# Kernel optimization log

Hardware: AMD Instinct MI355X
Metric: run time of the kernel (lower is better)

Reference implementation:

```python
import jax, jax.numpy as jnp
import numpy as np

N = 50000
E = 800000
IN_C, HID_C, OUT_C = 128, 128, 64


def setup_inputs() -> dict:
    key = jax.random.key(0)
    k_x, k_e, k_w1, k_w2 = jax.random.split(key, 4)
    x = jax.random.normal(k_x, (N, IN_C), dtype=jnp.float32)
    edge_index = jax.random.randint(k_e, (2, E), 0, N, dtype=jnp.int64)
    # glorot-ish init scale
    W1 = jax.random.normal(k_w1, (IN_C, HID_C), dtype=jnp.float32) * (1.0 / np.sqrt(IN_C))
    b1 = jnp.zeros((HID_C,), dtype=jnp.float32)
    W2 = jax.random.normal(k_w2, (HID_C, OUT_C), dtype=jnp.float32) * (1.0 / np.sqrt(HID_C))
    b2 = jnp.zeros((OUT_C,), dtype=jnp.float32)
    return {"x": x, "edge_index": edge_index, "W1": W1, "b1": b1, "W2": W2, "b2": b2}


def _gcn_norm(edge_index, num_nodes):
    # PyG gcn_norm with add_self_loops=True: deg over destination (col), sym norm
    loops = jnp.arange(num_nodes, dtype=edge_index.dtype)
    src = jnp.concatenate([edge_index[0], loops])
    dst = jnp.concatenate([edge_index[1], loops])
    deg = jax.ops.segment_sum(jnp.ones_like(dst, dtype=jnp.float32), dst, num_segments=num_nodes)
    dinv = jnp.where(deg > 0, jax.lax.rsqrt(deg), 0.0)
    norm = dinv[src] * dinv[dst]  # [E+N]
    return src, dst, norm


def _gcn_conv(x, src, dst, norm, W, b, num_nodes):
    h = x @ W                              # [N, out]
    msg = h[src] * norm[:, None]           # [E+N, out] gather + scale
    agg = jax.ops.segment_sum(msg, dst, num_segments=num_nodes)  # scatter-add
    return agg + b


def reference(x, edge_index, W1, b1, W2, b2):
    num_nodes = x.shape[0]
    src, dst, norm = _gcn_norm(edge_index, num_nodes)
    h = _gcn_conv(x, src, dst, norm, W1, b1, num_nodes)
    h = jax.nn.relu(h)
    out = _gcn_conv(h, src, dst, norm, W2, b2, num_nodes)
    return out
```

## Files before the change

### kernel.cpp

```cpp
#include <hip/hip_runtime.h>
#include <hip/hip_bf16.h>


#define IN_C 128
#define HID_C 128
#define OUT_C 64
#define BKT_SH 8
#define BKT_NODES 256
#define CHUNK 4096
#define CAPB 6144
#define OVF_CAP 65536

typedef float f32x4 __attribute__((ext_vector_type(4)));
typedef short bf16x8 __attribute__((ext_vector_type(8)));

__device__ inline unsigned short f2bf_rtn(float f) {
  unsigned u = __float_as_uint(f);
  unsigned r = u + 0x7fffu + ((u >> 16) & 1u);
  return (unsigned short)(r >> 16);
}
__device__ inline unsigned pack_bf2(float a, float b) {
  return (unsigned)f2bf_rtn(a) | ((unsigned)f2bf_rtn(b) << 16);
}

__global__ __launch_bounds__(256) void wt_zero_kernel(
    const float* __restrict__ W1, const float* __restrict__ W2,
    short* __restrict__ w1t, short* __restrict__ w2t,
    int* __restrict__ zbase, int zints) {
  int i = blockIdx.x * 256 + threadIdx.x;
  if (i < zints) zbase[i] = 0;
  if (i < IN_C * HID_C) {
    int n = i >> 7, k = i & 127;
    w1t[i] = (short)f2bf_rtn(W1[k * HID_C + n]);
  }
  if (i < HID_C * OUT_C) {
    int n = i >> 7, k = i & 127;
    w2t[i] = (short)f2bf_rtn(W2[k * OUT_C + n]);
  }
}

__global__ __launch_bounds__(256) void p1_gemm1_kernel(
    const int* __restrict__ ei, unsigned* __restrict__ pairs,
    int* __restrict__ bcnt, uint2* __restrict__ ovf, int* __restrict__ ovf_cnt,
    int* __restrict__ ovfb, int E, int K, int P1B,
    const float* __restrict__ X, const short* __restrict__ Wt,
    unsigned short* __restrict__ H, int ntiles) {
  int t = threadIdx.x;
  if ((int)blockIdx.x < P1B) {
    __shared__ unsigned buf[CHUNK];
    __shared__ int hist[256];
    __shared__ int lofs[256];
    __shared__ int cur[256];
    __shared__ int gbase[256];
    __shared__ int ws4[4];
    int base_e = blockIdx.x * CHUNK;
    int cnt_e = E - base_e;
    if (cnt_e > CHUNK) cnt_e = CHUNK;

    hist[t] = 0;
    __syncthreads();

    for (int i = t; i < cnt_e; i += 256)
      atomicAdd(&hist[ei[E + base_e + i] >> BKT_SH], 1);
    __syncthreads();

    int v = hist[t];
    int lane = t & 63, wid = t >> 6;
    int inc = v;
    #pragma unroll
    for (int off = 1; off < 64; off <<= 1) {
      int u = __shfl_up(inc, off, 64);
      if (lane >= off) inc += u;
    }
    if (lane == 63) ws4[wid] = inc;
    __syncthreads();
    if (t == 0) {
      int a = ws4[0], b = ws4[1], c = ws4[2];
      ws4[0] = 0; ws4[1] = a; ws4[2] = a + b; ws4[3] = a + b + c;
    }
    __syncthreads();
    int excl = ws4[wid] + inc - v;
    lofs[t] = excl;
    cur[t] = excl;
    if (t < K && v > 0) gbase[t] = atomicAdd(&bcnt[t], v);
    __syncthreads();

    for (int i = t; i < cnt_e; i += 256) {
      int src = ei[base_e + i];
      int dst = ei[E + base_e + i];
      int b = dst >> BKT_SH;
      int pos = atomicAdd(&cur[b], 1);
      buf[pos] = (unsigned)src | ((unsigned)(dst & (BKT_NODES - 1)) << 16) |
                 ((unsigned)b << 24);
    }
    __syncthreads();

    for (int i = t; i < cnt_e; i += 256) {
      unsigned w = buf[i];
      int b = w >> 24;
      int g = gbase[b] + (i - lofs[b]);
      if (g < CAPB) {
        pairs[(size_t)b * CAPB + g] = w;
      } else {
        int oi = atomicAdd(ovf_cnt, 1);
        if (oi < OVF_CAP) {
          unsigned dst = (unsigned)(b << BKT_SH) | ((w >> 16) & 0xFFu);
          ovf[oi] = make_uint2(w & 0xFFFFu, dst);
          atomicAdd(&ovfb[b], 1);
        }
      }
    }
  } else {
    int lane = t & 63;
    int tile = ((int)blockIdx.x - P1B) * 4 + (t >> 6);
    if (tile >= ntiles) return;
    constexpr int NT = HID_C / 16;

    int arow = tile * 16 + (lane & 15);
    int kch = (lane >> 4) * 8;

    bf16x8 afrag[4];
    const float4* Xf = (const float4*)X;
    #pragma unroll
    for (int kt = 0; kt < 4; ++kt) {
      float4 f0 = Xf[(size_t)arow * 32 + (kt * 32 + kch) / 4];
      float4 f1 = Xf[(size_t)arow * 32 + (kt * 32 + kch) / 4 + 1];
      bf16x8 a;
      a[0] = (short)f2bf_rtn(f0.x); a[1] = (short)f2bf_rtn(f0.y);
      a[2] = (short)f2bf_rtn(f0.z); a[3] = (short)f2bf_rtn(f0.w);
      a[4] = (short)f2bf_rtn(f1.x); a[5] = (short)f2bf_rtn(f1.y);
      a[6] = (short)f2bf_rtn(f1.z); a[7] = (short)f2bf_rtn(f1.w);
      afrag[kt] = a;
    }

    const bf16x8* W8 = (const bf16x8*)Wt;
    f32x4 zero = {0.f, 0.f, 0.f, 0.f};
    f32x4 acc[NT];
    #pragma unroll
    for (int ct = 0; ct < NT; ++ct) acc[ct] = zero;

    #pragma unroll
    for (int ct = 0; ct < NT; ++ct) {
      int bcol = ct * 16 + (lane & 15);
      #pragma unroll
      for (int kt = 0; kt < 4; ++kt) {
        bf16x8 b = W8[bcol * 16 + (kt * 32 + kch) / 8];
        acc[ct] = __builtin_amdgcn_mfma_f32_16x16x32_bf16(afrag[kt], b, acc[ct], 0, 0, 0);
      }
    }

    int r0 = tile * 16 + (lane >> 4) * 4;
    #pragma unroll
    for (int ct = 0; ct < NT; ++ct) {
      #pragma unroll
      for (int j = 0; j < 4; ++j)
        H[(size_t)(r0 + j) * HID_C + ct * 16 + (lane & 15)] = f2bf_rtn(acc[ct][j]);
    }
  }
}

__global__ __launch_bounds__(256) void phase2_csr_kernel(
    const unsigned* __restrict__ pairs, const int* __restrict__ bcnt,
    const int* __restrict__ ovfb, const uint2* __restrict__ ovf,
    const int* __restrict__ ovf_cnt, int* __restrict__ rowstart,
    float* __restrict__ dinv, unsigned short* __restrict__ csr, int N, int K) {
  int b = blockIdx.x;
  int t = threadIdx.x;
  __shared__ int hist[BKT_NODES];
  __shared__ int cur[BKT_NODES];
  __shared__ int sbase[256];
  __shared__ int ws4[4];
  int lane = t & 63, wid = t >> 6;

  int cb = 0;
  if (t < K) {
    int c = bcnt[t];
    cb = (c < CAPB ? c : CAPB) + ovfb[t];
  }
  {
    int inc = cb;
    #pragma unroll
    for (int off = 1; off < 64; off <<= 1) {
      int u = __shfl_up(inc, off, 64);
      if (lane >= off) inc += u;
    }
    if (lane == 63) ws4[wid] = inc;
    __syncthreads();
    if (t == 0) {
      int a = ws4[0], bb = ws4[1], c = ws4[2];
      ws4[0] = 0; ws4[1] = a; ws4[2] = a + bb; ws4[3] = a + bb + c;
    }
    __syncthreads();
    int excl = ws4[wid] + inc - cb;
    sbase[t] = excl;
    if (b == K - 1 && t == K - 1) rowstart[N] = excl + cb;
  }
  __syncthreads();
  int base = sbase[b];

  hist[t] = 0;
  __syncthreads();

  int cnt = bcnt[b];
  if (cnt > CAPB) cnt = CAPB;
  const unsigned* reg = pairs + (size_t)b * CAPB;

  for (int i = t; i < cnt; i += 256)
    atomicAdd(&hist[(reg[i] >> 16) & 0xFFu], 1);
  int oc = *ovf_cnt;
  if (oc > OVF_CAP) oc = OVF_CAP;
  for (int i = t; i < oc; i += 256) {
    uint2 p = ovf[i];
    if ((int)(p.y >> BKT_SH) == b) atomicAdd(&hist[p.y & (BKT_NODES - 1)], 1);
  }
  __syncthreads();

  int v = hist[t];
  int inc = v;
  #pragma unroll
  for (int off = 1; off < 64; off <<= 1) {
    int u = __shfl_up(inc, off, 64);
    if (lane >= off) inc += u;
  }
  __syncthreads();
  if (lane == 63) ws4[wid] = inc;
  __syncthreads();
  if (t == 0) {
    int a = ws4[0], bb = ws4[1], c = ws4[2];
    ws4[0] = 0; ws4[1] = a; ws4[2] = a + bb; ws4[3] = a + bb + c;
  }
  __syncthreads();
  int excl = ws4[wid] + inc - v;

  int node = b * BKT_NODES + t;
  if (node < N) {
    rowstart[node] = base + excl;
    dinv[node] = rsqrtf((float)(v + 1));
  }
  cur[t] = base + excl;
  __syncthreads();

  for (int i = t; i < cnt; i += 256) {
    unsigned w = reg[i];
    int pos = atomicAdd(&cur[(w >> 16) & 0xFFu], 1);
    csr[pos] = (unsigned short)(w & 0xffffu);
  }
  for (int i = t; i < oc; i += 256) {
    uint2 p = ovf[i];
    if ((int)(p.y >> BKT_SH) == b) {
      int pos = atomicAdd(&cur[p.y & (BKT_NODES - 1)], 1);
      csr[pos] = (unsigned short)p.x;
    }
  }
}

__global__ __launch_bounds__(256) void mfma_gemm2_kernel(
    const unsigned short* __restrict__ Xb16, const short* __restrict__ Wt,
    const float* __restrict__ dinv, unsigned short* __restrict__ H, int ntiles) {
  int lane = threadIdx.x & 63;
  int tile = blockIdx.x * 4 + (threadIdx.x >> 6);
  if (tile >= ntiles) return;
  constexpr int NT = OUT_C / 16;

  int arow = tile * 16 + (lane & 15);
  int kch = (lane >> 4) * 8;

  const bf16x8* Xb = (const bf16x8*)Xb16;
  bf16x8 afrag[4];
  #pragma unroll
  for (int kt = 0; kt < 4; ++kt)
    afrag[kt] = Xb[(size_t)arow * 16 + (kt * 32 + kch) / 8];

  const bf16x8* W8 = (const bf16x8*)Wt;
  f32x4 zero = {0.f, 0.f, 0.f, 0.f};
  f32x4 acc[NT];
  #pragma unroll
  for (int ct = 0; ct < NT; ++ct) acc[ct] = zero;

  #pragma unroll
  for (int ct = 0; ct < NT; ++ct) {
    int bcol = ct * 16 + (lane & 15);
    #pragma unroll
    for (int kt = 0; kt < 4; ++kt) {
      bf16x8 b = W8[bcol * 16 + (kt * 32 + kch) / 8];
      acc[ct] = __builtin_amdgcn_mfma_f32_16x16x32_bf16(afrag[kt], b, acc[ct], 0, 0, 0);
    }
  }

  int r0 = tile * 16 + (lane >> 4) * 4;
  float di[4];
  #pragma unroll
  for (int j = 0; j < 4; ++j) di[j] = dinv[r0 + j];
  #pragma unroll
  for (int ct = 0; ct < NT; ++ct) {
    #pragma unroll
    for (int j = 0; j < 4; ++j)
      H[(size_t)(r0 + j) * OUT_C + ct * 16 + (lane & 15)] = f2bf_rtn(acc[ct][j] * di[j]);
  }
}

template <int C, bool RELU, bool OUT_BF16, bool SRC_SCALE>
__global__ __launch_bounds__(256) void agg_bf16_kernel(
    const unsigned short* __restrict__ Hs, const int* __restrict__ rowstart,
    const unsigned short* __restrict__ csr, const float* __restrict__ dinv,
    const float* __restrict__ bias, void* __restrict__ out, int n) {
  constexpr int TPN = C / 8;
  constexpr int NPB = 256 / TPN;
  int lane = threadIdx.x % TPN;
  int node = blockIdx.x * NPB + threadIdx.x / TPN;
  if (node >= n) return;

  const uint4* H4 = reinterpret_cast<const uint4*>(Hs);
  int s = rowstart[node];
  int e = rowstart[node + 1];
  float dnode = dinv[node];

  float acc[8];
  {
    uint4 v = H4[(size_t)node * TPN + lane];
    float ds = SRC_SCALE ? dnode : 1.0f;
    acc[0] = __uint_as_float(v.x << 16) * ds;
    acc[1] = __uint_as_float(v.x & 0xffff0000u) * ds;
    acc[2] = __uint_as_float(v.y << 16) * ds;
    acc[3] = __uint_as_float(v.y & 0xffff0000u) * ds;
    acc[4] = __uint_as_float(v.z << 16) * ds;
    acc[5] = __uint_as_float(v.z & 0xffff0000u) * ds;
    acc[6] = __uint_as_float(v.w << 16) * ds;
    acc[7] = __uint_as_float(v.w & 0xffff0000u) * ds;
  }

  int p = s;
  for (; p + 1 < e; p += 2) {
    int s0 = csr[p];
    int s1 = csr[p + 1];
    uint4 v0 = H4[(size_t)s0 * TPN + lane];
    uint4 v1 = H4[(size_t)s1 * TPN + lane];
    if (SRC_SCALE) {
      float d0 = dinv[s0], d1 = dinv[s1];
      acc[0] = fmaf(__uint_as_float(v0.x << 16), d0, acc[0]);
      acc[1] = fmaf(__uint_as_float(v0.x & 0xffff0000u), d0, acc[1]);
      acc[2] = fmaf(__uint_as_float(v0.y << 16), d0, acc[2]);
      acc[3] = fmaf(__uint_as_float(v0.y & 0xffff0000u), d0, acc[3]);
      acc[4] = fmaf(__uint_as_float(v0.z << 16), d0, acc[4]);
      acc[5] = fmaf(__uint_as_float(v0.z & 0xffff0000u), d0, acc[5]);
      acc[6] = fmaf(__uint_as_float(v0.w << 16), d0, acc[6]);
      acc[7] = fmaf(__uint_as_float(v0.w & 0xffff0000u), d0, acc[7]);
      acc[0] = fmaf(__uint_as_float(v1.x << 16), d1, acc[0]);
      acc[1] = fmaf(__uint_as_float(v1.x & 0xffff0000u), d1, acc[1]);
      acc[2] = fmaf(__uint_as_float(v1.y << 16), d1, acc[2]);
      acc[3] = fmaf(__uint_as_float(v1.y & 0xffff0000u), d1, acc[3]);
      acc[4] = fmaf(__uint_as_float(v1.z << 16), d1, acc[4]);
      acc[5] = fmaf(__uint_as_float(v1.z & 0xffff0000u), d1, acc[5]);
      acc[6] = fmaf(__uint_as_float(v1.w << 16), d1, acc[6]);
      acc[7] = fmaf(__uint_as_float(v1.w & 0xffff0000u), d1, acc[7]);
    } else {
      acc[0] += __uint_as_float(v0.x << 16);
      acc[1] += __uint_as_float(v0.x & 0xffff0000u);
      acc[2] += __uint_as_float(v0.y << 16);
      acc[3] += __uint_as_float(v0.y & 0xffff0000u);
      acc[4] += __uint_as_float(v0.z << 16);
      acc[5] += __uint_as_float(v0.z & 0xffff0000u);
      acc[6] += __uint_as_float(v0.w << 16);
      acc[7] += __uint_as_float(v0.w & 0xffff0000u);
      acc[0] += __uint_as_float(v1.x << 16);
      acc[1] += __uint_as_float(v1.x & 0xffff0000u);
      acc[2] += __uint_as_float(v1.y << 16);
      acc[3] += __uint_as_float(v1.y & 0xffff0000u);
      acc[4] += __uint_as_float(v1.z << 16);
      acc[5] += __uint_as_float(v1.z & 0xffff0000u);
      acc[6] += __uint_as_float(v1.w << 16);
      acc[7] += __uint_as_float(v1.w & 0xffff0000u);
    }
  }
  if (p < e) {
    int s0 = csr[p];
    uint4 v0 = H4[(size_t)s0 * TPN + lane];
    float d0 = SRC_SCALE ? dinv[s0] : 1.0f;
    acc[0] = fmaf(__uint_as_float(v0.x << 16), d0, acc[0]);
    acc[1] = fmaf(__uint_as_float(v0.x & 0xffff0000u), d0, acc[1]);
    acc[2] = fmaf(__uint_as_float(v0.y << 16), d0, acc[2]);
    acc[3] = fmaf(__uint_as_float(v0.y & 0xffff0000u), d0, acc[3]);
    acc[4] = fmaf(__uint_as_float(v0.z << 16), d0, acc[4]);
    acc[5] = fmaf(__uint_as_float(v0.z & 0xffff0000u), d0, acc[5]);
    acc[6] = fmaf(__uint_as_float(v0.w << 16), d0, acc[6]);
    acc[7] = fmaf(__uint_as_float(v0.w & 0xffff0000u), d0, acc[7]);
  }

  float4 b0 = reinterpret_cast<const float4*>(bias)[lane * 2];
  float4 b1 = reinterpret_cast<const float4*>(bias)[lane * 2 + 1];
  float r[8];
  r[0] = fmaf(acc[0], dnode, b0.x);
  r[1] = fmaf(acc[1], dnode, b0.y);
  r[2] = fmaf(acc[2], dnode, b0.z);
  r[3] = fmaf(acc[3], dnode, b0.w);
  r[4] = fmaf(acc[4], dnode, b1.x);
  r[5] = fmaf(acc[5], dnode, b1.y);
  r[6] = fmaf(acc[6], dnode, b1.z);
  r[7] = fmaf(acc[7], dnode, b1.w);
  if (RELU) {
    #pragma unroll
    for (int j = 0; j < 8; ++j) r[j] = fmaxf(r[j], 0.f);
  }
  if (OUT_BF16) {
    uint4 o;
    o.x = pack_bf2(r[0], r[1]);
    o.y = pack_bf2(r[2], r[3]);
    o.z = pack_bf2(r[4], r[5]);
    o.w = pack_bf2(r[6], r[7]);
    reinterpret_cast<uint4*>(out)[(size_t)node * TPN + lane] = o;
  } else {
    float4* o4 = reinterpret_cast<float4*>(out) + (size_t)node * (C / 4);
    o4[lane * 2] = make_float4(r[0], r[1], r[2], r[3]);
    o4[lane * 2 + 1] = make_float4(r[4], r[5], r[6], r[7]);
  }
}

extern "C" void kernel_launch(void* const* d_in, const int* in_sizes, int n_in,
                              void* d_out, int out_size, void* d_ws, size_t ws_size,
                              hipStream_t stream) {
  const float* x  = (const float*)d_in[0];
  const int*   ei = (const int*)d_in[1];
  const float* W1 = (const float*)d_in[2];
  const float* b1 = (const float*)d_in[3];
  const float* W2 = (const float*)d_in[4];
  const float* b2 = (const float*)d_in[5];
  float* out = (float*)d_out;

  const int N = in_sizes[0] / IN_C;
  const int E = in_sizes[1] / 2;
  const int K = (N + BKT_NODES - 1) >> BKT_SH;
  const int NTILES = (N + 15) / 16;
  const int P1B = (E + CHUNK - 1) / CHUNK;
  const int GB1 = (NTILES + 3) / 4;

  char* ws = (char*)d_ws;
  size_t off = 0;
  auto alloc = [&](size_t bytes) -> void* {
    void* p = ws + off;
    off += (bytes + 255) & ~(size_t)255;
    return p;
  };
  int* bcnt    = (int*)alloc((size_t)K * 4);
  int* ovf_cnt = (int*)alloc(4);
  int* ovfb    = (int*)alloc((size_t)K * 4);
  size_t zero_bytes = off;
  const int zints = (int)(zero_bytes / 4);

  int*   rowstart    = (int*)  alloc((size_t)(N + 1) * 4);
  float* dinv        = (float*)alloc((size_t)N * 4);
  unsigned* pairs    = (unsigned*)alloc((size_t)K * CAPB * 4);
  uint2* ovf         = (uint2*)alloc((size_t)OVF_CAP * 8);
  unsigned short* csr = (unsigned short*)alloc((size_t)E * 2);
  unsigned short* hs  = (unsigned short*)alloc((size_t)N * HID_C * 2);
  unsigned short* x2  = (unsigned short*)alloc((size_t)N * HID_C * 2);
  short* w1t         = (short*)alloc((size_t)IN_C * HID_C * 2);
  short* w2t         = (short*)alloc((size_t)HID_C * OUT_C * 2);

  int wt_threads = zints > IN_C * HID_C ? zints : IN_C * HID_C;
  wt_zero_kernel<<<(wt_threads + 255) / 256, 256, 0, stream>>>(
      W1, W2, w1t, w2t, (int*)ws, zints);

  p1_gemm1_kernel<<<P1B + GB1, 256, 0, stream>>>(
      ei, pairs, bcnt, ovf, ovf_cnt, ovfb, E, K, P1B, x, w1t, hs, NTILES);

  phase2_csr_kernel<<<K, 256, 0, stream>>>(
      pairs, bcnt, ovfb, ovf, ovf_cnt, rowstart, dinv, csr, N, K);

  agg_bf16_kernel<HID_C, true, true, true><<<(N + 15) / 16, 256, 0, stream>>>(
      hs, rowstart, csr, dinv, b1, x2, N);

  mfma_gemm2_kernel<<<(NTILES + 3) / 4, 256, 0, stream>>>(
      x2, w2t, dinv, hs, NTILES);

  agg_bf16_kernel<OUT_C, false, false, false><<<(N + 31) / 32, 256, 0, stream>>>(
      hs, rowstart, csr, dinv, b2, out, N);
}
```

Baseline: 110.5 us.

## Fuse layer-1 aggregation with layer-2 MFMA GEMM via shared memory tile

Layer-1 aggregation (with ReLU and bias) now feeds a 16-row bf16 tile held in LDS directly into the layer-2 MFMA GEMM inside one kernel. This drops the N×128 bf16 intermediate write and read-back, plus one kernel launch. Each of the four waves computes one 16-column output tile. The cost is a block-wide sync after the irregular gather, so each block waits on its slowest node and the GEMM stage sees lower occupancy and latency hiding.

```diff
diff --git a/kernel.cpp b/kernel.cpp
--- a/kernel.cpp
+++ b/kernel.cpp
@@ -254,88 +254,45 @@
   }
 }
 
-__global__ __launch_bounds__(256) void mfma_gemm2_kernel(
-    const unsigned short* __restrict__ Xb16, const short* __restrict__ Wt,
-    const float* __restrict__ dinv, unsigned short* __restrict__ H, int ntiles) {
-  int lane = threadIdx.x & 63;
-  int tile = blockIdx.x * 4 + (threadIdx.x >> 6);
-  if (tile >= ntiles) return;
-  constexpr int NT = OUT_C / 16;
-
-  int arow = tile * 16 + (lane & 15);
-  int kch = (lane >> 4) * 8;
-
-  const bf16x8* Xb = (const bf16x8*)Xb16;
-  bf16x8 afrag[4];
-  #pragma unroll
-  for (int kt = 0; kt < 4; ++kt)
-    afrag[kt] = Xb[(size_t)arow * 16 + (kt * 32 + kch) / 8];
-
-  const bf16x8* W8 = (const bf16x8*)Wt;
-  f32x4 zero = {0.f, 0.f, 0.f, 0.f};
-  f32x4 acc[NT];
-  #pragma unroll
-  for (int ct = 0; ct < NT; ++ct) acc[ct] = zero;
-
-  #pragma unroll
-  for (int ct = 0; ct < NT; ++ct) {
-    int bcol = ct * 16 + (lane & 15);
-    #pragma unroll
-    for (int kt = 0; kt < 4; ++kt) {
-      bf16x8 b = W8[bcol * 16 + (kt * 32 + kch) / 8];
-      acc[ct] = __builtin_amdgcn_mfma_f32_16x16x32_bf16(afrag[kt], b, acc[ct], 0, 0, 0);
-    }
-  }
-
-  int r0 = tile * 16 + (lane >> 4) * 4;
-  float di[4];
-  #pragma unroll
-  for (int j = 0; j < 4; ++j) di[j] = dinv[r0 + j];
-  #pragma unroll
-  for (int ct = 0; ct < NT; ++ct) {
-    #pragma unroll
-    for (int j = 0; j < 4; ++j)
-      H[(size_t)(r0 + j) * OUT_C + ct * 16 + (lane & 15)] = f2bf_rtn(acc[ct][j] * di[j]);
-  }
-}
-
-template <int C, bool RELU, bool OUT_BF16, bool SRC_SCALE>
-__global__ __launch_bounds__(256) void agg_bf16_kernel(
+__global__ __launch_bounds__(256) void agg1_gemm2_kernel(
     const unsigned short* __restrict__ Hs, const int* __restrict__ rowstart,
     const unsigned short* __restrict__ csr, const float* __restrict__ dinv,
-    const float* __restrict__ bias, void* __restrict__ out, int n) {
-  constexpr int TPN = C / 8;
-  constexpr int NPB = 256 / TPN;
-  int lane = threadIdx.x % TPN;
-  int node = blockIdx.x * NPB + threadIdx.x / TPN;
-  if (node >= n) return;
-
-  const uint4* H4 = reinterpret_cast<const uint4*>(Hs);
-  int s = rowstart[node];
-  int e = rowstart[node + 1];
-  float dnode = dinv[node];
+    const float* __restrict__ b1, const short* __restrict__ w2t,
+    unsigned short* __restrict__ H2, int n) {
+  __shared__ unsigned x2s[16][64];
+  int t = threadIdx.x;
+  int row = t >> 4;
+  int lane16 = t & 15;
+  int node = blockIdx.x * 16 + row;
 
   float acc[8];
-  {
-    uint4 v = H4[(size_t)node * TPN + lane];
-    float ds = SRC_SCALE ? dnode : 1.0f;
-    acc[0] = __uint_as_float(v.x << 16) * ds;
-    acc[1] = __uint_as_float(v.x & 0xffff0000u) * ds;
-    acc[2] = __uint_as_float(v.y << 16) * ds;
-    acc[3] = __uint_as_float(v.y & 0xffff0000u) * ds;
-    acc[4] = __uint_as_float(v.z << 16) * ds;
-    acc[5] = __uint_as_float(v.z & 0xffff0000u) * ds;
-    acc[6] = __uint_as_float(v.w << 16) * ds;
-    acc[7] = __uint_as_float(v.w & 0xffff0000u) * ds;
-  }
-
-  int p = s;
-  for (; p + 1 < e; p += 2) {
-    int s0 = csr[p];
-    int s1 = csr[p + 1];
-    uint4 v0 = H4[(size_t)s0 * TPN + lane];
-    uint4 v1 = H4[(size_t)s1 * TPN + lane];
-    if (SRC_SCALE) {
+  #pragma unroll
+  for (int j = 0; j < 8; ++j) acc[j] = 0.f;
+
+  if (node < n) {
+    const uint4* H4 = reinterpret_cast<const uint4*>(Hs);
+    int s = rowstart[node];
+    int e = rowstart[node + 1];
+    float dnode = dinv[node];
+
+    {
+      uint4 v = H4[(size_t)node * 16 + lane16];
+      acc[0] = __uint_as_float(v.x << 16) * dnode;
+      acc[1] = __uint_as_float(v.x & 0xffff0000u) * dnode;
+      acc[2] = __uint_as_float(v.y << 16) * dnode;
+      acc[3] = __uint_as_float(v.y & 0xffff0000u) * dnode;
+      acc[4] = __uint_as_float(v.z << 16) * dnode;
+      acc[5] = __uint_as_float(v.z & 0xffff0000u) * dnode;
+      acc[6] = __uint_as_float(v.w << 16) * dnode;
+      acc[7] = __uint_as_float(v.w & 0xffff0000u) * dnode;
+    }
+
+    int p = s;
+    for (; p + 1 < e; p += 2) {
+      int s0 = csr[p];
+      int s1 = csr[p + 1];
+      uint4 v0 = H4[(size_t)s0 * 16 + lane16];
+      uint4 v1 = H4[(size_t)s1 * 16 + lane16];
       float d0 = dinv[s0], d1 = dinv[s1];
       acc[0] = fmaf(__uint_as_float(v0.x << 16), d0, acc[0]);
       acc[1] = fmaf(__uint_as_float(v0.x & 0xffff0000u), d0, acc[1]);
@@ -353,66 +310,134 @@
       acc[5] = fmaf(__uint_as_float(v1.z & 0xffff0000u), d1, acc[5]);
       acc[6] = fmaf(__uint_as_float(v1.w << 16), d1, acc[6]);
       acc[7] = fmaf(__uint_as_float(v1.w & 0xffff0000u), d1, acc[7]);
-    } else {
-      acc[0] += __uint_as_float(v0.x << 16);
-      acc[1] += __uint_as_float(v0.x & 0xffff0000u);
-      acc[2] += __uint_as_float(v0.y << 16);
-      acc[3] += __uint_as_float(v0.y & 0xffff0000u);
-      acc[4] += __uint_as_float(v0.z << 16);
-      acc[5] += __uint_as_float(v0.z & 0xffff0000u);
-      acc[6] += __uint_as_float(v0.w << 16);
-      acc[7] += __uint_as_float(v0.w & 0xffff0000u);
-      acc[0] += __uint_as_float(v1.x << 16);
-      acc[1] += __uint_as_float(v1.x & 0xffff0000u);
-      acc[2] += __uint_as_float(v1.y << 16);
-      acc[3] += __uint_as_float(v1.y & 0xffff0000u);
-      acc[4] += __uint_as_float(v1.z << 16);
-      acc[5] += __uint_as_float(v1.z & 0xffff0000u);
-      acc[6] += __uint_as_float(v1.w << 16);
-      acc[7] += __uint_as_float(v1.w & 0xffff0000u);
-    }
+    }
+    if (p < e) {
+      int s0 = csr[p];
+      uint4 v0 = H4[(size_t)s0 * 16 + lane16];
+      float d0 = dinv[s0];
+      acc[0] = fmaf(__uint_as_float(v0.x << 16), d0, acc[0]);
+      acc[1] = fmaf(__uint_as_float(v0.x & 0xffff0000u), d0, acc[1]);
+      acc[2] = fmaf(__uint_as_float(v0.y << 16), d0, acc[2]);
+      acc[3] = fmaf(__uint_as_float(v0.y & 0xffff0000u), d0, acc[3]);
+      acc[4] = fmaf(__uint_as_float(v0.z << 16), d0, acc[4]);
+      acc[5] = fmaf(__uint_as_float(v0.z & 0xffff0000u), d0, acc[5]);
+      acc[6] = fmaf(__uint_as_float(v0.w << 16), d0, acc[6]);
+      acc[7] = fmaf(__uint_as_float(v0.w & 0xffff0000u), d0, acc[7]);
+    }
+
+    const float4* b4 = reinterpret_cast<const float4*>(b1);
+    float4 bv0 = b4[lane16 * 2];
+    float4 bv1 = b4[lane16 * 2 + 1];
+    acc[0] = fmaxf(fmaf(acc[0], dnode, bv0.x), 0.f);
+    acc[1] = fmaxf(fmaf(acc[1], dnode, bv0.y), 0.f);
+    acc[2] = fmaxf(fmaf(acc[2], dnode, bv0.z), 0.f);
+    acc[3] = fmaxf(fmaf(acc[3], dnode, bv0.w), 0.f);
+    acc[4] = fmaxf(fmaf(acc[4], dnode, bv1.x), 0.f);
+    acc[5] = fmaxf(fmaf(acc[5], dnode, bv1.y), 0.f);
+    acc[6] = fmaxf(fmaf(acc[6], dnode, bv1.z), 0.f);
+    acc[7] = fmaxf(fmaf(acc[7], dnode, bv1.w), 0.f);
+  }
+
+  x2s[row][lane16 * 4 + 0] = pack_bf2(acc[0], acc[1]);
+  x2s[row][lane16 * 4 + 1] = pack_bf2(acc[2], acc[3]);
+  x2s[row][lane16 * 4 + 2] = pack_bf2(acc[4], acc[5]);
+  x2s[row][lane16 * 4 + 3] = pack_bf2(acc[6], acc[7]);
+  __syncthreads();
+
+  int lane = t & 63;
+  int w = t >> 6;
+  int kch = (lane >> 4) * 8;
+
+  const bf16x8* W8 = (const bf16x8*)w2t;
+  f32x4 oacc = {0.f, 0.f, 0.f, 0.f};
+  int bcol = w * 16 + (lane & 15);
+  #pragma unroll
+  for (int kt = 0; kt < 4; ++kt) {
+    bf16x8 a = *reinterpret_cast<const bf16x8*>(&x2s[lane & 15][kt * 16 + kch / 2]);
+    bf16x8 b = W8[bcol * 16 + (kt * 32 + kch) / 8];
+    oacc = __builtin_amdgcn_mfma_f32_16x16x32_bf16(a, b, oacc, 0, 0, 0);
+  }
+
+  int r0 = (lane >> 4) * 4;
+  #pragma unroll
+  for (int j = 0; j < 4; ++j) {
+    int g = blockIdx.x * 16 + r0 + j;
+    if (g < n)
+      H2[(size_t)g * OUT_C + w * 16 + (lane & 15)] = f2bf_rtn(oacc[j] * dinv[g]);
+  }
+}
+
+__global__ __launch_bounds__(256) void agg2_kernel(
+    const unsigned short* __restrict__ Hs, const int* __restrict__ rowstart,
+    const unsigned short* __restrict__ csr, const float* __restrict__ dinv,
+    const float* __restrict__ bias, float* __restrict__ out, int n) {
+  constexpr int TPN = OUT_C / 8;
+  constexpr int NPB = 256 / TPN;
+  int lane = threadIdx.x % TPN;
+  int node = blockIdx.x * NPB + threadIdx.x / TPN;
+  if (node >= n) return;
+
+  const uint4* H4 = reinterpret_cast<const uint4*>(Hs);
+  int s = rowstart[node];
+  int e = rowstart[node + 1];
+
+  float acc[8];
+  {
+    uint4 v = H4[(size_t)node * TPN + lane];
+    acc[0] = __uint_as_float(v.x << 16);
+    acc[1] = __uint_as_float(v.x & 0xffff0000u);
+    acc[2] = __uint_as_float(v.y << 16);
+    acc[3] = __uint_as_float(v.y & 0xffff0000u);
+    acc[4] = __uint_as_float(v.z << 16);
+    acc[5] = __uint_as_float(v.z & 0xffff0000u);
+    acc[6] = __uint_as_float(v.w << 16);
+    acc[7] = __uint_as_float(v.w & 0xffff0000u);
+  }
+
+  int p = s;
+  for (; p + 1 < e; p += 2) {
+    int s0 = csr[p];
+    int s1 = csr[p + 1];
+    uint4 v0 = H4[(size_t)s0 * TPN + lane];
+    uint4 v1 = H4[(size_t)s1 * TPN + lane];
+    acc[0] += __uint_as_float(v0.x << 16);
+    acc[1] += __uint_as_float(v0.x & 0xffff0000u);
+    acc[2] += __uint_as_float(v0.y << 16);
+    acc[3] += __uint_as_float(v0.y & 0xffff0000u);
+    acc[4] += __uint_as_float(v0.z << 16);
+    acc[5] += __uint_as_float(v0.z & 0xffff0000u);
+    acc[6] += __uint_as_float(v0.w << 16);
+    acc[7] += __uint_as_float(v0.w & 0xffff0000u);
+    acc[0] += __uint_as_float(v1.x << 16);
+    acc[1] += __uint_as_float(v1.x & 0xffff0000u);
+    acc[2] += __uint_as_float(v1.y << 16);
+    acc[3] += __uint_as_float(v1.y & 0xffff0000u);
+    acc[4] += __uint_as_float(v1.z << 16);
+    acc[5] += __uint_as_float(v1.z & 0xffff0000u);
+    acc[6] += __uint_as_float(v1.w << 16);
+    acc[7] += __uint_as_float(v1.w & 0xffff0000u);
   }
   if (p < e) {
     int s0 = csr[p];
     uint4 v0 = H4[(size_t)s0 * TPN + lane];
-    float d0 = SRC_SCALE ? dinv[s0] : 1.0f;
-    acc[0] = fmaf(__uint_as_float(v0.x << 16), d0, acc[0]);
-    acc[1] = fmaf(__uint_as_float(v0.x & 0xffff0000u), d0, acc[1]);
-    acc[2] = fmaf(__uint_as_float(v0.y << 16), d0, acc[2]);
-    acc[3] = fmaf(__uint_as_float(v0.y & 0xffff0000u), d0, acc[3]);
-    acc[4] = fmaf(__uint_as_float(v0.z << 16), d0, acc[4]);
-    acc[5] = fmaf(__uint_as_float(v0.z & 0xffff0000u), d0, acc[5]);
-    acc[6] = fmaf(__uint_as_float(v0.w << 16), d0, acc[6]);
-    acc[7] = fmaf(__uint_as_float(v0.w & 0xffff0000u), d0, acc[7]);
-  }
-
+    acc[0] += __uint_as_float(v0.x << 16);
+    acc[1] += __uint_as_float(v0.x & 0xffff0000u);
+    acc[2] += __uint_as_float(v0.y << 16);
+    acc[3] += __uint_as_float(v0.y & 0xffff0000u);
+    acc[4] += __uint_as_float(v0.z << 16);
+    acc[5] += __uint_as_float(v0.z & 0xffff0000u);
+    acc[6] += __uint_as_float(v0.w << 16);
+    acc[7] += __uint_as_float(v0.w & 0xffff0000u);
+  }
+
+  float dnode = dinv[node];
   float4 b0 = reinterpret_cast<const float4*>(bias)[lane * 2];
   float4 b1 = reinterpret_cast<const float4*>(bias)[lane * 2 + 1];
-  float r[8];
-  r[0] = fmaf(acc[0], dnode, b0.x);
-  r[1] = fmaf(acc[1], dnode, b0.y);
-  r[2] = fmaf(acc[2], dnode, b0.z);
-  r[3] = fmaf(acc[3], dnode, b0.w);
-  r[4] = fmaf(acc[4], dnode, b1.x);
-  r[5] = fmaf(acc[5], dnode, b1.y);
-  r[6] = fmaf(acc[6], dnode, b1.z);
-  r[7] = fmaf(acc[7], dnode, b1.w);
-  if (RELU) {
-    #pragma unroll
-    for (int j = 0; j < 8; ++j) r[j] = fmaxf(r[j], 0.f);
-  }
-  if (OUT_BF16) {
-    uint4 o;
-    o.x = pack_bf2(r[0], r[1]);
-    o.y = pack_bf2(r[2], r[3]);
-    o.z = pack_bf2(r[4], r[5]);
-    o.w = pack_bf2(r[6], r[7]);
-    reinterpret_cast<uint4*>(out)[(size_t)node * TPN + lane] = o;
-  } else {
-    float4* o4 = reinterpret_cast<float4*>(out) + (size_t)node * (C / 4);
-    o4[lane * 2] = make_float4(r[0], r[1], r[2], r[3]);
-    o4[lane * 2 + 1] = make_float4(r[4], r[5], r[6], r[7]);
-  }
+  float4* o4 = reinterpret_cast<float4*>(out) + (size_t)node * (OUT_C / 4);
+  o4[lane * 2] = make_float4(fmaf(acc[0], dnode, b0.x), fmaf(acc[1], dnode, b0.y),
+                             fmaf(acc[2], dnode, b0.z), fmaf(acc[3], dnode, b0.w));
+  o4[lane * 2 + 1] = make_float4(fmaf(acc[4], dnode, b1.x), fmaf(acc[5], dnode, b1.y),
+                                 fmaf(acc[6], dnode, b1.z), fmaf(acc[7], dnode, b1.w));
 }
 
 extern "C" void kernel_launch(void* const* d_in, const int* in_sizes, int n_in,
@@ -452,7 +477,7 @@
   uint2* ovf         = (uint2*)alloc((size_t)OVF_CAP * 8);
   unsigned short* csr = (unsigned short*)alloc((size_t)E * 2);
   unsigned short* hs  = (unsigned short*)alloc((size_t)N * HID_C * 2);
-  unsigned short* x2  = (unsigned short*)alloc((size_t)N * HID_C * 2);
+  unsigned short* hs2 = (unsigned short*)alloc((size_t)N * OUT_C * 2);
   short* w1t         = (short*)alloc((size_t)IN_C * HID_C * 2);
   short* w2t         = (short*)alloc((size_t)HID_C * OUT_C * 2);
 
@@ -466,12 +491,9 @@
   phase2_csr_kernel<<<K, 256, 0, stream>>>(
       pairs, bcnt, ovfb, ovf, ovf_cnt, rowstart, dinv, csr, N, K);
 
-  agg_bf16_kernel<HID_C, true, true, true><<<(N + 15) / 16, 256, 0, stream>>>(
-      hs, rowstart, csr, dinv, b1, x2, N);
-
-  mfma_gemm2_kernel<<<(NTILES + 3) / 4, 256, 0, stream>>>(
-      x2, w2t, dinv, hs, NTILES);
-
-  agg_bf16_kernel<OUT_C, false, false, false><<<(N + 31) / 32, 256, 0, stream>>>(
-      hs, rowstart, csr, dinv, b2, out, N);
-}
+  agg1_gemm2_kernel<<<NTILES, 256, 0, stream>>>(
+      hs, rowstart, csr, dinv, b1, w2t, hs2, N);
+
+  agg2_kernel<<<(N + 31) / 32, 256, 0, stream>>>(
+      hs2, rowstart, csr, dinv, b2, out, N);
+}
```

New measurement: 102.9 us. 6.9% less time.
